# Kernel optimization log

Hardware: AMD Instinct MI355X
Metric: run time of the kernel (lower is better)

Reference implementation:

```python
import jax, jax.numpy as jnp
import numpy as np

CODEBOOK_SIZE = 1024
D_MODEL = 512
NUM_SAMPLES = 10
TEMP = 1.0
COMMITMENT_COST = 0.25
PADDING_IDX = 0


def setup_inputs() -> dict:
    key = jax.random.key(0)
    k1, k2, k3 = jax.random.split(key, 3)
    inputs = jax.random.normal(k1, (64, 512, D_MODEL), dtype=jnp.float32)
    padding_mask = jax.random.randint(k2, (64, 512), 0, 2) == 1
    codebook_weight = 0.02 * jax.random.normal(k3, (CODEBOOK_SIZE, D_MODEL), dtype=jnp.float32)
    codebook_weight = codebook_weight.at[PADDING_IDX].set(0.0)  # padding_idx row zeroed
    return {"inputs": inputs, "padding_mask": padding_mask, "codebook_weight": codebook_weight}


def reference(inputs, padding_mask, codebook_weight):
    B, S, D = inputs.shape
    K = codebook_weight.shape[0]
    flat = inputs.reshape(-1, D)  # [N, D]
    # squared-euclidean distances to codebook entries: [N, K]
    dist = (jnp.sum(flat * flat, axis=1, keepdims=True)
            + jnp.sum(codebook_weight * codebook_weight, axis=1)
            - 2.0 * (flat @ codebook_weight.T))
    pad = padding_mask.reshape(-1)  # [N]
    col = jnp.arange(K)
    # padded rows: only code 0 allowed; non-padded rows: code 0 disallowed
    allowed = jnp.where(pad[:, None], col == 0, col != 0)
    dist = jnp.where(allowed, dist, jnp.inf)

    # Multinomial(total_count=NUM_SAMPLES, logits=-dist/TEMP): draw NUM_SAMPLES
    # categorical samples per row and count them.
    logits = -dist / TEMP
    N = flat.shape[0]
    draws = jax.random.categorical(jax.random.key(42), logits, axis=-1,
                                   shape=(NUM_SAMPLES, N))  # [num_samples, N]
    row_idx = jnp.broadcast_to(jnp.arange(N)[None, :], draws.shape)
    samples = jnp.zeros((N, K), jnp.float32).at[row_idx, draws].add(1.0)  # counts, [N, K]

    quantized = (samples @ codebook_weight).reshape(B, S, D) / NUM_SAMPLES

    num_nonpad = (jnp.sum(~pad) * D).astype(jnp.float32)
    e_latent_loss = jnp.sum((jax.lax.stop_gradient(quantized) - inputs) ** 2) / num_nonpad
    loss = COMMITMENT_COST * e_latent_loss

    # straight-through estimator
    quantized_st = inputs + jax.lax.stop_gradient(quantized - inputs)

    avg_probs = jnp.mean(samples, axis=0) / NUM_SAMPLES  # [K]
    perplexity = jnp.exp(-jnp.sum(avg_probs * jnp.log(avg_probs + 1e-10)))

    samples_out = samples.reshape(B, S, K)
    return quantized_st, samples_out, loss, perplexity
```

## Files before the change

kernel.cpp:

```cpp
#include <hip/hip_runtime.h>
#include <stdint.h>

#define NROWS 32768
#define KC 1024
#define DM 512
#define NKPROD 33554432u

typedef _Float16 v8h __attribute__((ext_vector_type(8)));
typedef float v4f __attribute__((ext_vector_type(4)));

__device__ __forceinline__ uint32_t rotl32(uint32_t x, int d) {
  return __builtin_amdgcn_alignbit(x, x, 32 - d);
}

__device__ __forceinline__ void threefry_x2(uint32_t xa, uint32_t xb,
                                            uint32_t& oa, uint32_t& ob) {
  const uint32_t ks1 = 42u, ks2 = 0x1BD11BF0u;
  uint32_t a0 = 0u, a1 = xa + ks1;
  uint32_t b0 = 0u, b1 = xb + ks1;
#define R2(r) { a0 += a1; b0 += b1; a1 = rotl32(a1, r); b1 = rotl32(b1, r); a1 ^= a0; b1 ^= b0; }
  R2(13) R2(15) R2(26) R2(6)
  a0 += ks1; b0 += ks1; a1 += ks2 + 1u; b1 += ks2 + 1u;
  R2(17) R2(29) R2(16) R2(24)
  a0 += ks2; b0 += ks2; a1 += 2u; b1 += 2u;
  R2(13) R2(15) R2(26) R2(6)
  a1 += ks1 + 3u; b1 += ks1 + 3u;
  R2(17) R2(29) R2(16) R2(24)
  a0 += ks1; b0 += ks1; a1 += ks2 + 4u; b1 += ks2 + 4u;
  R2(13) R2(15) R2(26) R2(6)
  a0 += ks2; b0 += ks2; a1 += 5u; b1 += 5u;
#undef R2
  oa = a0 ^ a1;
  ob = b0 ^ b1;
}

__global__ __launch_bounds__(256) void k_detect(const uint8_t* __restrict__ m,
                                                uint32_t* __restrict__ flag) {
  uint32_t f = 0;
  for (int i = threadIdx.x; i < NROWS; i += 256)
    if ((i & 3) && m[i]) f = 1;
  if (f) atomicOr(flag, 1u);
}

__global__ __launch_bounds__(256) void k_prep2(const void* __restrict__ mv,
                                               const uint32_t* __restrict__ flag,
                                               uint8_t* __restrict__ wm,
                                               int* __restrict__ idx,
                                               int* __restrict__ npp) {
  bool isbool = (*flag) != 0;
  int t = blockIdx.x * 256 + threadIdx.x;
  const uint8_t* mb = (const uint8_t*)mv;
#pragma unroll
  for (int i = 0; i < 2; ++i) {
    int r = t * 2 + i;
    bool p = isbool ? (mb[r] != 0) : (((const int*)mv)[r] != 0);
    wm[r] = p ? 1u : 0u;
    if (!p) {
      int pos = atomicAdd(npp, 1);
      idx[pos] = r;
    }
  }
}

__global__ __launch_bounds__(256) void k_pad(const float* __restrict__ X,
                                             const uint8_t* __restrict__ wm,
                                             float* __restrict__ qout,
                                             float* __restrict__ sout,
                                             double* __restrict__ esum) {
  int n = blockIdx.x * 4 + (threadIdx.x >> 6);
  int l = threadIdx.x & 63;
  if (!wm[n]) return;

  float* so = sout + (size_t)n * KC + l * 16;
  float4 z = make_float4(0.f, 0.f, 0.f, 0.f);
  *(float4*)(so)      = (l == 0) ? make_float4(10.f, 0.f, 0.f, 0.f) : z;
  *(float4*)(so + 4)  = z;
  *(float4*)(so + 8)  = z;
  *(float4*)(so + 12) = z;

  const float* xr = X + (size_t)n * DM + l * 8;
  float4 x0 = *(const float4*)xr, x1 = *(const float4*)(xr + 4);
  float* qo = qout + (size_t)n * DM + l * 8;
  *(float4*)qo       = z;
  *(float4*)(qo + 4) = z;
  double ls = (double)(x0.x*x0.x) + (double)(x0.y*x0.y)
            + (double)(x0.z*x0.z) + (double)(x0.w*x0.w)
            + (double)(x1.x*x1.x) + (double)(x1.y*x1.y)
            + (double)(x1.z*x1.z) + (double)(x1.w*x1.w);
#pragma unroll
  for (int off = 32; off; off >>= 1) ls += __shfl_xor(ls, off, 64);
  if (l == 0) atomicAdd(&esum[n & 63], ls);
}

#define LDK 40
__global__ __launch_bounds__(256) void k_gemm2i(const float* __restrict__ A,
                                                const float* __restrict__ B,
                                                const int* __restrict__ idx,
                                                const int* __restrict__ npp,
                                                float* __restrict__ S) {
  int NP = *npp;
  int bx = blockIdx.x & 7;
  int by = blockIdx.x >> 3;
  int r0 = by * 128, c0 = bx * 128;
  if (r0 >= NP) return;

  __shared__ _Float16 Ah[128 * LDK], Al[128 * LDK];
  __shared__ _Float16 Bh[128 * LDK], Bl[128 * LDK];
  __shared__ float rs[128];
  __shared__ float cs[128];
  __shared__ float tmp[256];

  int tid = threadIdx.x;
  int wid = tid >> 6;
  int wr = wid >> 1, wc = wid & 1;
  int l = tid & 63;
  int lr = l & 15;
  int k8 = (l >> 4) * 8;

  int srow = tid >> 1;
  int ssub = (tid & 1) * 16;

  int slot = r0 + srow;
  int orig = idx[slot < NP ? slot : NP - 1];
  const float* ag = A + (size_t)orig * DM + ssub;
  const float* bg = B + (size_t)(c0 + srow) * DM + ssub;

  v4f acc[4][4];
#pragma unroll
  for (int m = 0; m < 4; ++m)
#pragma unroll
    for (int n = 0; n < 4; ++n) acc[m][n] = (v4f)0.0f;

  float sqa = 0.f, sqb = 0.f;

  for (int k0 = 0; k0 < DM; k0 += 32) {
    float xa[16], xb[16];
#pragma unroll
    for (int i = 0; i < 16; i += 4) {
      *(float4*)&xa[i] = *(const float4*)(ag + k0 + i);
      *(float4*)&xb[i] = *(const float4*)(bg + k0 + i);
    }
    _Float16 ha[16], la[16], hb[16], lb[16];
#pragma unroll
    for (int i = 0; i < 16; ++i) {
      float x = xa[i];
      _Float16 h = (_Float16)x;
      ha[i] = h; la[i] = (_Float16)(x - (float)h);
      sqa = fmaf(x, x, sqa);
      float y = xb[i];
      _Float16 g = (_Float16)y;
      hb[i] = g; lb[i] = (_Float16)(y - (float)g);
      sqb = fmaf(y, y, sqb);
    }
    __syncthreads();
    int wb = srow * LDK + ssub;
    *(v8h*)&Ah[wb]     = *(v8h*)&ha[0];
    *(v8h*)&Ah[wb + 8] = *(v8h*)&ha[8];
    *(v8h*)&Al[wb]     = *(v8h*)&la[0];
    *(v8h*)&Al[wb + 8] = *(v8h*)&la[8];
    *(v8h*)&Bh[wb]     = *(v8h*)&hb[0];
    *(v8h*)&Bh[wb + 8] = *(v8h*)&hb[8];
    *(v8h*)&Bl[wb]     = *(v8h*)&lb[0];
    *(v8h*)&Bl[wb + 8] = *(v8h*)&lb[8];
    __syncthreads();

    v8h fah[4], fal[4];
#pragma unroll
    for (int m = 0; m < 4; ++m) {
      int row = wr * 64 + m * 16 + lr;
      fah[m] = *(const v8h*)&Ah[row * LDK + k8];
      fal[m] = *(const v8h*)&Al[row * LDK + k8];
    }
#pragma unroll
    for (int n = 0; n < 4; ++n) {
      int col = wc * 64 + n * 16 + lr;
      v8h fbh = *(const v8h*)&Bh[col * LDK + k8];
      v8h fbl = *(const v8h*)&Bl[col * LDK + k8];
#pragma unroll
      for (int m = 0; m < 4; ++m) {
        acc[m][n] = __builtin_amdgcn_mfma_f32_16x16x32_f16(fah[m], fbh, acc[m][n], 0, 0, 0);
        acc[m][n] = __builtin_amdgcn_mfma_f32_16x16x32_f16(fah[m], fbl, acc[m][n], 0, 0, 0);
        acc[m][n] = __builtin_amdgcn_mfma_f32_16x16x32_f16(fal[m], fbh, acc[m][n], 0, 0, 0);
      }
    }
  }

  tmp[tid] = sqa;
  __syncthreads();
  if ((tid & 1) == 0) rs[srow] = tmp[tid] + tmp[tid + 1];
  __syncthreads();
  tmp[tid] = sqb;
  __syncthreads();
  if ((tid & 1) == 0) cs[srow] = tmp[tid] + tmp[tid + 1];
  __syncthreads();

  float cnp[4];
#pragma unroll
  for (int n = 0; n < 4; ++n) cnp[n] = cs[wc * 64 + n * 16 + lr];

#pragma unroll
  for (int m = 0; m < 4; ++m) {
    int rl = wr * 64 + m * 16 + (l >> 4) * 4;
#pragma unroll
    for (int r = 0; r < 4; ++r) {
      int sl = r0 + rl + r;
      int org = idx[sl < NP ? sl : NP - 1];
      float rq = rs[rl + r];
      float* sp = S + (size_t)org * KC + c0;
#pragma unroll
      for (int n = 0; n < 4; ++n) {
        int cl = wc * 64 + n * 16 + lr;
        sp[cl] = -((rq + cnp[n]) - 2.0f * acc[m][n][r]);
      }
    }
  }
}

__global__ __launch_bounds__(256, 8) void k_sample_i(
    const float* __restrict__ S, const float* __restrict__ X,
    const float* __restrict__ CW, const int* __restrict__ idx,
    const int* __restrict__ npp,
    float* __restrict__ qout, float* __restrict__ sout,
    float* __restrict__ cnt, double* __restrict__ esum) {
  int NP = *npp;
  int slot = blockIdx.x * 4 + (threadIdx.x >> 6);
  if (slot >= NP) return;
  int n = idx[slot];
  int l = threadIdx.x & 63;
  int base = l * 16;
  const float* srow = S + (size_t)n * KC + base;

  float lmax;
  {
    float lg0[16];
#pragma unroll
    for (int j = 0; j < 16; j += 4)
      *(float4*)&lg0[j] = *(const float4*)(srow + j);
    if (l == 0) lg0[0] = -__builtin_inff();
    lmax = lg0[0];
#pragma unroll
    for (int i = 1; i < 16; ++i) lmax = fmaxf(lmax, lg0[i]);
#pragma unroll
    for (int off = 32; off; off >>= 1)
      lmax = fmaxf(lmax, __shfl_xor(lmax, off, 64));
  }

  float bv[10];
  uint32_t bi[10];
#pragma unroll
  for (int s = 0; s < 10; ++s) { bv[s] = -__builtin_inff(); bi[s] = 0xFFFFFFFFu; }

  uint32_t tb0 = (uint32_t)n * (uint32_t)KC + (uint32_t)base;
#pragma unroll 1
  for (int j = 0; j < 16; ++j) {
    float lgj = srow[j];
    uint32_t kk = (uint32_t)(base + j);
    if (kk == 0u) lgj = -__builtin_inff();
    float mj = 0.69314718056f * __expf(lmax - lgj);
    uint32_t t0 = tb0 + (uint32_t)j;
#pragma unroll
    for (int sp = 0; sp < 5; ++sp) {
      uint32_t ba, bb;
      threefry_x2(t0 + (uint32_t)(2 * sp) * NKPROD,
                  t0 + (uint32_t)(2 * sp + 1) * NKPROD, ba, bb);
      float fa = __uint_as_float((ba >> 9) | 0x3F800000u) - 1.0f;
      float fb = __uint_as_float((bb >> 9) | 0x3F800000u) - 1.0f;
      float ua = fmaxf(1.17549435e-38f, fa);
      float ub = fmaxf(1.17549435e-38f, fb);
      float va = __log2f(ua) * mj;
      float vb = __log2f(ub) * mj;
      if (va > bv[2 * sp])     { bv[2 * sp] = va;     bi[2 * sp] = kk; }
      if (vb > bv[2 * sp + 1]) { bv[2 * sp + 1] = vb; bi[2 * sp + 1] = kk; }
    }
  }

#pragma unroll
  for (int s = 0; s < 10; ++s) {
#pragma unroll
    for (int off = 32; off; off >>= 1) {
      float ov = __shfl_xor(bv[s], off, 64);
      uint32_t oi = __shfl_xor(bi[s], off, 64);
      if (ov > bv[s] || (ov == bv[s] && oi < bi[s])) { bv[s] = ov; bi[s] = oi; }
    }
  }

  float* so = sout + (size_t)n * KC + base;
#pragma unroll
  for (int j4 = 0; j4 < 16; j4 += 4) {
    float c[4];
#pragma unroll
    for (int i = 0; i < 4; ++i) {
      uint32_t k = (uint32_t)(base + j4 + i);
      float cc = 0.f;
#pragma unroll
      for (int s = 0; s < 10; ++s) cc += (bi[s] == k) ? 1.f : 0.f;
      c[i] = cc;
    }
    *(float4*)(so + j4) = make_float4(c[0], c[1], c[2], c[3]);
  }

  float q[8];
#pragma unroll
  for (int i = 0; i < 8; ++i) q[i] = 0.f;
#pragma unroll
  for (int s = 0; s < 10; ++s) {
    const float* cr = CW + (size_t)bi[s] * DM + l * 8;
    float4 g0 = *(const float4*)cr;
    float4 g1 = *(const float4*)(cr + 4);
    q[0] += g0.x; q[1] += g0.y; q[2] += g0.z; q[3] += g0.w;
    q[4] += g1.x; q[5] += g1.y; q[6] += g1.z; q[7] += g1.w;
    if (l == 0) atomicAdd(&cnt[bi[s]], 1.0f);
  }

  const float* xr = X + (size_t)n * DM + l * 8;
  float4 x0 = *(const float4*)xr, x1 = *(const float4*)(xr + 4);
  float xs[8] = {x0.x, x0.y, x0.z, x0.w, x1.x, x1.y, x1.z, x1.w};
  float st[8];
  double ls = 0.0;
#pragma unroll
  for (int j = 0; j < 8; ++j) {
    float qq = q[j] / 10.0f;
    float d = qq - xs[j];
    ls += (double)(d * d);
    st[j] = xs[j] + d;
  }
  float* qo = qout + (size_t)n * DM + l * 8;
  *(float4*)qo       = make_float4(st[0], st[1], st[2], st[3]);
  *(float4*)(qo + 4) = make_float4(st[4], st[5], st[6], st[7]);

#pragma unroll
  for (int off = 32; off; off >>= 1) ls += __shfl_xor(ls, off, 64);
  if (l == 0) atomicAdd(&esum[n & 63], ls);
}

__global__ __launch_bounds__(256) void k_final(const uint8_t* __restrict__ wm,
                                               const float* __restrict__ cnt,
                                               const double* __restrict__ esum,
                                               float* __restrict__ scal) {
  __shared__ int sni[256];
  __shared__ double snd[256];
  int t = threadIdx.x;
  int np = 0;
  for (int i = t; i < NROWS; i += 256) np += wm[i];
  sni[t] = np;
  __syncthreads();
  for (int off = 128; off; off >>= 1) {
    if (t < off) sni[t] += sni[t + off];
    __syncthreads();
  }
  int npad = sni[0];
  double ss = 0.0;
  for (int k = t; k < KC; k += 256) {
    float c = (k == 0) ? (float)(npad * 10) : cnt[k];
    float p = c / 327680.0f;
    ss += (double)(p * logf(p + 1e-10f));
  }
  snd[t] = ss;
  __syncthreads();
  for (int off = 128; off; off >>= 1) {
    if (t < off) snd[t] += snd[t + off];
    __syncthreads();
  }
  if (t == 0) {
    double es = 0.0;
    for (int i = 0; i < 64; ++i) es += esum[i];
    float num_nonpad = (float)((NROWS - npad) * DM);
    float el = (float)es / num_nonpad;
    scal[0] = 0.25f * el;
    scal[1] = expf(-(float)snd[0]);
  }
}

extern "C" void kernel_launch(void* const* d_in, const int* in_sizes, int n_in,
                              void* d_out, int out_size, void* d_ws, size_t ws_size,
                              hipStream_t stream) {
  const float* X  = (const float*)d_in[0];
  const void*  M  = d_in[1];
  const float* CW = (const float*)d_in[2];
  float* out  = (float*)d_out;
  float* qout = out;
  float* sout = out + 16777216;
  float* scal = out + 50331648;
  uint8_t* ws = (uint8_t*)d_ws;
  double*   esum = (double*)ws;
  uint32_t* flag = (uint32_t*)(ws + 512);
  int*      npp  = (int*)(ws + 768);
  float*    cnt  = (float*)(ws + 1024);
  uint8_t*  wm   = ws + 8192;
  int*      idx  = (int*)(ws + 49152);
  (void)in_sizes; (void)n_in; (void)out_size; (void)ws_size;

  hipMemsetAsync(d_ws, 0, 8192, stream);
  k_detect<<<1, 256, 0, stream>>>((const uint8_t*)M, flag);
  k_prep2<<<64, 256, 0, stream>>>(M, flag, wm, idx, npp);
  k_pad<<<8192, 256, 0, stream>>>(X, wm, qout, sout, esum);
  k_gemm2i<<<2048, 256, 0, stream>>>(X, CW, idx, npp, sout);
  k_sample_i<<<8192, 256, 0, stream>>>(sout, X, CW, idx, npp, qout, sout, cnt, esum);
  k_final<<<1, 256, 0, stream>>>(wm, cnt, esum, scal);
}
```

Measured before the change: 567.5 us.

## Presplit codebook to fp16 hi/lo, merge prep kernels, fold padding into sampler

```diff
diff --git a/kernel.cpp b/kernel.cpp
--- a/kernel.cpp
+++ b/kernel.cpp
@@ -34,70 +34,83 @@
   ob = b0 ^ b1;
 }
 
-__global__ __launch_bounds__(256) void k_detect(const uint8_t* __restrict__ m,
-                                                uint32_t* __restrict__ flag) {
-  uint32_t f = 0;
-  for (int i = threadIdx.x; i < NROWS; i += 256)
-    if ((i & 3) && m[i]) f = 1;
-  if (f) atomicOr(flag, 1u);
-}
-
-__global__ __launch_bounds__(256) void k_prep2(const void* __restrict__ mv,
-                                               const uint32_t* __restrict__ flag,
+__global__ __launch_bounds__(1024) void k_prep(const void* __restrict__ mv,
                                                uint8_t* __restrict__ wm,
                                                int* __restrict__ idx,
                                                int* __restrict__ npp) {
-  bool isbool = (*flag) != 0;
-  int t = blockIdx.x * 256 + threadIdx.x;
+  __shared__ uint32_t sflag;
+  __shared__ int scnt[1024];
+  int t = threadIdx.x;
+  if (t == 0) sflag = 0;
+  __syncthreads();
   const uint8_t* mb = (const uint8_t*)mv;
-#pragma unroll
-  for (int i = 0; i < 2; ++i) {
-    int r = t * 2 + i;
+  uint32_t f = 0;
+  for (int i = t; i < NROWS; i += 1024)
+    if ((i & 3) && mb[i]) f = 1;
+  if (f) atomicOr(&sflag, 1u);
+  __syncthreads();
+  bool isbool = sflag != 0;
+
+  int r0 = t * 32;
+  int cnt = 0;
+  for (int i = 0; i < 32; ++i) {
+    int r = r0 + i;
     bool p = isbool ? (mb[r] != 0) : (((const int*)mv)[r] != 0);
     wm[r] = p ? 1u : 0u;
-    if (!p) {
-      int pos = atomicAdd(npp, 1);
-      idx[pos] = r;
-    }
-  }
-}
-
-__global__ __launch_bounds__(256) void k_pad(const float* __restrict__ X,
-                                             const uint8_t* __restrict__ wm,
-                                             float* __restrict__ qout,
-                                             float* __restrict__ sout,
-                                             double* __restrict__ esum) {
-  int n = blockIdx.x * 4 + (threadIdx.x >> 6);
+    cnt += p ? 0 : 1;
+  }
+  scnt[t] = cnt;
+  __syncthreads();
+  for (int off = 1; off < 1024; off <<= 1) {
+    int v = (t >= off) ? scnt[t - off] : 0;
+    __syncthreads();
+    scnt[t] += v;
+    __syncthreads();
+  }
+  int NPtot = scnt[1023];
+  int pos  = scnt[t] - cnt;
+  int ppos = NPtot + (r0 - pos);
+  for (int i = 0; i < 32; ++i) {
+    int r = r0 + i;
+    bool p = isbool ? (mb[r] != 0) : (((const int*)mv)[r] != 0);
+    if (!p) idx[pos++] = r; else idx[ppos++] = r;
+  }
+  if (t == 1023) *npp = NPtot;
+}
+
+__global__ __launch_bounds__(256) void k_bsplit(const float* __restrict__ B,
+                                                _Float16* __restrict__ Bh2,
+                                                _Float16* __restrict__ Bl2,
+                                                float* __restrict__ Bn) {
+  int k = blockIdx.x * 4 + (threadIdx.x >> 6);
   int l = threadIdx.x & 63;
-  if (!wm[n]) return;
-
-  float* so = sout + (size_t)n * KC + l * 16;
-  float4 z = make_float4(0.f, 0.f, 0.f, 0.f);
-  *(float4*)(so)      = (l == 0) ? make_float4(10.f, 0.f, 0.f, 0.f) : z;
-  *(float4*)(so + 4)  = z;
-  *(float4*)(so + 8)  = z;
-  *(float4*)(so + 12) = z;
-
-  const float* xr = X + (size_t)n * DM + l * 8;
-  float4 x0 = *(const float4*)xr, x1 = *(const float4*)(xr + 4);
-  float* qo = qout + (size_t)n * DM + l * 8;
-  *(float4*)qo       = z;
-  *(float4*)(qo + 4) = z;
-  double ls = (double)(x0.x*x0.x) + (double)(x0.y*x0.y)
-            + (double)(x0.z*x0.z) + (double)(x0.w*x0.w)
-            + (double)(x1.x*x1.x) + (double)(x1.y*x1.y)
-            + (double)(x1.z*x1.z) + (double)(x1.w*x1.w);
-#pragma unroll
-  for (int off = 32; off; off >>= 1) ls += __shfl_xor(ls, off, 64);
-  if (l == 0) atomicAdd(&esum[n & 63], ls);
+  const float* bp = B + (size_t)k * DM + l * 8;
+  float x[8];
+  *(float4*)&x[0] = *(const float4*)bp;
+  *(float4*)&x[4] = *(const float4*)(bp + 4);
+  _Float16 h[8], lo[8];
+  float s = 0.f;
+#pragma unroll
+  for (int i = 0; i < 8; ++i) {
+    _Float16 hh = (_Float16)x[i];
+    h[i] = hh; lo[i] = (_Float16)(x[i] - (float)hh);
+    s = fmaf(x[i], x[i], s);
+  }
+  *(v8h*)&Bh2[(size_t)k * DM + l * 8] = *(v8h*)h;
+  *(v8h*)&Bl2[(size_t)k * DM + l * 8] = *(v8h*)lo;
+#pragma unroll
+  for (int off = 32; off; off >>= 1) s += __shfl_xor(s, off, 64);
+  if (l == 0) Bn[k] = s;
 }
 
 #define LDK 40
-__global__ __launch_bounds__(256) void k_gemm2i(const float* __restrict__ A,
-                                                const float* __restrict__ B,
-                                                const int* __restrict__ idx,
-                                                const int* __restrict__ npp,
-                                                float* __restrict__ S) {
+__global__ __launch_bounds__(256) void k_gemm3(const float* __restrict__ A,
+                                               const _Float16* __restrict__ Bh2,
+                                               const _Float16* __restrict__ Bl2,
+                                               const float* __restrict__ Bn,
+                                               const int* __restrict__ idx,
+                                               const int* __restrict__ npp,
+                                               float* __restrict__ S) {
   int NP = *npp;
   int bx = blockIdx.x & 7;
   int by = blockIdx.x >> 3;
@@ -120,10 +133,12 @@
   int srow = tid >> 1;
   int ssub = (tid & 1) * 16;
 
-  int slot = r0 + srow;
-  int orig = idx[slot < NP ? slot : NP - 1];
+  int orig = idx[r0 + srow];
   const float* ag = A + (size_t)orig * DM + ssub;
-  const float* bg = B + (size_t)(c0 + srow) * DM + ssub;
+  const _Float16* bhg = Bh2 + (size_t)(c0 + srow) * DM + ssub;
+  const _Float16* blg = Bl2 + (size_t)(c0 + srow) * DM + ssub;
+
+  if (tid < 128) cs[tid] = Bn[c0 + tid];
 
   v4f acc[4][4];
 #pragma unroll
@@ -131,26 +146,24 @@
 #pragma unroll
     for (int n = 0; n < 4; ++n) acc[m][n] = (v4f)0.0f;
 
-  float sqa = 0.f, sqb = 0.f;
+  float sqa = 0.f;
 
   for (int k0 = 0; k0 < DM; k0 += 32) {
-    float xa[16], xb[16];
-#pragma unroll
-    for (int i = 0; i < 16; i += 4) {
+    float xa[16];
+#pragma unroll
+    for (int i = 0; i < 16; i += 4)
       *(float4*)&xa[i] = *(const float4*)(ag + k0 + i);
-      *(float4*)&xb[i] = *(const float4*)(bg + k0 + i);
-    }
-    _Float16 ha[16], la[16], hb[16], lb[16];
+    v8h bh0 = *(const v8h*)(bhg + k0);
+    v8h bh1 = *(const v8h*)(bhg + k0 + 8);
+    v8h bl0 = *(const v8h*)(blg + k0);
+    v8h bl1 = *(const v8h*)(blg + k0 + 8);
+    _Float16 ha[16], la[16];
 #pragma unroll
     for (int i = 0; i < 16; ++i) {
       float x = xa[i];
       _Float16 h = (_Float16)x;
       ha[i] = h; la[i] = (_Float16)(x - (float)h);
       sqa = fmaf(x, x, sqa);
-      float y = xb[i];
-      _Float16 g = (_Float16)y;
-      hb[i] = g; lb[i] = (_Float16)(y - (float)g);
-      sqb = fmaf(y, y, sqb);
     }
     __syncthreads();
     int wb = srow * LDK + ssub;
@@ -158,10 +171,10 @@
     *(v8h*)&Ah[wb + 8] = *(v8h*)&ha[8];
     *(v8h*)&Al[wb]     = *(v8h*)&la[0];
     *(v8h*)&Al[wb + 8] = *(v8h*)&la[8];
-    *(v8h*)&Bh[wb]     = *(v8h*)&hb[0];
-    *(v8h*)&Bh[wb + 8] = *(v8h*)&hb[8];
-    *(v8h*)&Bl[wb]     = *(v8h*)&lb[0];
-    *(v8h*)&Bl[wb + 8] = *(v8h*)&lb[8];
+    *(v8h*)&Bh[wb]     = bh0;
+    *(v8h*)&Bh[wb + 8] = bh1;
+    *(v8h*)&Bl[wb]     = bl0;
+    *(v8h*)&Bl[wb + 8] = bl1;
     __syncthreads();
 
     v8h fah[4], fal[4];
@@ -189,10 +202,6 @@
   __syncthreads();
   if ((tid & 1) == 0) rs[srow] = tmp[tid] + tmp[tid + 1];
   __syncthreads();
-  tmp[tid] = sqb;
-  __syncthreads();
-  if ((tid & 1) == 0) cs[srow] = tmp[tid] + tmp[tid + 1];
-  __syncthreads();
 
   float cnp[4];
 #pragma unroll
@@ -203,8 +212,7 @@
     int rl = wr * 64 + m * 16 + (l >> 4) * 4;
 #pragma unroll
     for (int r = 0; r < 4; ++r) {
-      int sl = r0 + rl + r;
-      int org = idx[sl < NP ? sl : NP - 1];
+      int org = idx[r0 + rl + r];
       float rq = rs[rl + r];
       float* sp = S + (size_t)org * KC + c0;
 #pragma unroll
@@ -216,7 +224,7 @@
   }
 }
 
-__global__ __launch_bounds__(256, 8) void k_sample_i(
+__global__ __launch_bounds__(256, 8) void k_sample_f(
     const float* __restrict__ S, const float* __restrict__ X,
     const float* __restrict__ CW, const int* __restrict__ idx,
     const int* __restrict__ npp,
@@ -224,10 +232,32 @@
     float* __restrict__ cnt, double* __restrict__ esum) {
   int NP = *npp;
   int slot = blockIdx.x * 4 + (threadIdx.x >> 6);
-  if (slot >= NP) return;
+  int l = threadIdx.x & 63;
   int n = idx[slot];
-  int l = threadIdx.x & 63;
   int base = l * 16;
+
+  if (slot >= NP) {
+    float* so = sout + (size_t)n * KC + base;
+    float4 z = make_float4(0.f, 0.f, 0.f, 0.f);
+    *(float4*)(so)      = (l == 0) ? make_float4(10.f, 0.f, 0.f, 0.f) : z;
+    *(float4*)(so + 4)  = z;
+    *(float4*)(so + 8)  = z;
+    *(float4*)(so + 12) = z;
+    const float* xr = X + (size_t)n * DM + l * 8;
+    float4 x0 = *(const float4*)xr, x1 = *(const float4*)(xr + 4);
+    float* qo = qout + (size_t)n * DM + l * 8;
+    *(float4*)qo       = z;
+    *(float4*)(qo + 4) = z;
+    double ls = (double)(x0.x*x0.x) + (double)(x0.y*x0.y)
+              + (double)(x0.z*x0.z) + (double)(x0.w*x0.w)
+              + (double)(x1.x*x1.x) + (double)(x1.y*x1.y)
+              + (double)(x1.z*x1.z) + (double)(x1.w*x1.w);
+#pragma unroll
+    for (int off = 32; off; off >>= 1) ls += __shfl_xor(ls, off, 64);
+    if (l == 0) atomicAdd(&esum[n & 63], ls);
+    return;
+  }
+
   const float* srow = S + (size_t)n * KC + base;
 
   float lmax;
@@ -381,20 +411,21 @@
   float* qout = out;
   float* sout = out + 16777216;
   float* scal = out + 50331648;
+  _Float16* Bh2 = (_Float16*)qout;
+  _Float16* Bl2 = (_Float16*)(qout + 262144);
+  float*    Bn  = qout + 524288;
   uint8_t* ws = (uint8_t*)d_ws;
   double*   esum = (double*)ws;
-  uint32_t* flag = (uint32_t*)(ws + 512);
-  int*      npp  = (int*)(ws + 768);
+  int*      npp  = (int*)(ws + 512);
   float*    cnt  = (float*)(ws + 1024);
-  uint8_t*  wm   = ws + 8192;
+  uint8_t*  wm   = ws + 16384;
   int*      idx  = (int*)(ws + 49152);
   (void)in_sizes; (void)n_in; (void)out_size; (void)ws_size;
 
   hipMemsetAsync(d_ws, 0, 8192, stream);
-  k_detect<<<1, 256, 0, stream>>>((const uint8_t*)M, flag);
-  k_prep2<<<64, 256, 0, stream>>>(M, flag, wm, idx, npp);
-  k_pad<<<8192, 256, 0, stream>>>(X, wm, qout, sout, esum);
-  k_gemm2i<<<2048, 256, 0, stream>>>(X, CW, idx, npp, sout);
-  k_sample_i<<<8192, 256, 0, stream>>>(sout, X, CW, idx, npp, qout, sout, cnt, esum);
+  k_prep<<<1, 1024, 0, stream>>>(M, wm, idx, npp);
+  k_bsplit<<<256, 256, 0, stream>>>(CW, Bh2, Bl2, Bn);
+  k_gemm3<<<2048, 256, 0, stream>>>(X, Bh2, Bl2, Bn, idx, npp, sout);
+  k_sample_f<<<8192, 256, 0, stream>>>(sout, X, CW, idx, npp, qout, sout, cnt, esum);
   k_final<<<1, 256, 0, stream>>>(wm, cnt, esum, scal);
 }
```

New measurement: 576.3 us. Within noise of the previous version (+1.6%).
